# Kernel optimization log

Hardware: AMD Instinct MI355X
Metric: run time of the kernel (lower is better)

## Reference

```python
import jax, jax.numpy as jnp
import numpy as np

# Flattened-state gather indices. State is prev[9,3] flattened to 27 values,
# then concat with x -> flat[29], where flat[27]=a=x[0], flat[28]=b=x[1].
# Row t gives the (x0, x1, x2) inputs of triangle t, read from the source wiring.
IDX0 = np.array([3, 0, 6, 12, 9, 15, 18, 6, 15])   # x0 inputs
IDX1 = np.array([1, 7, 4, 19, 16, 13, 10, 22, 25])  # x1 inputs
IDX2 = np.array([17, 5, 11, 8, 28, 2, 27, 23, 26])  # x2 inputs (t=4 -> b, t=6 -> a)

NOISE_SCALE = 0.125  # LUT2 hard-codes noise = 0.125


def mux(s, a, b):
    return 0.5 * (s * b - s * a + a + b)


def setup_inputs() -> dict:
    key = jax.random.key(0)
    k1, k2, k3 = jax.random.split(key, 3)
    x = jax.random.normal(k1, (2,), dtype=jnp.float32)
    weights = jax.random.normal(k2, (9, 3, 4), dtype=jnp.float32)  # 9 triangles x 3 LUT2s x 4 weights
    noise = jax.random.normal(k3, (130, 9, 3, 4), dtype=jnp.float32)  # per-step np.random.normal draws
    return {"x": x, "weights": weights, "noise": noise, "dummy1": 0, "dummy2": 0}


def reference(x, weights, noise, dummy1, dummy2):
    del dummy1, dummy2  # unused in the original forward

    def step(prev, n):
        # prev: [9,3] current states; n: [9,3,4] noise for this step
        flat = jnp.concatenate([prev.reshape(-1), x])  # [29]
        x0, x1, x2 = flat[IDX0], flat[IDX1], flat[IDX2]  # each [9]
        # LUT j of each triangle: LUT0(x1,x2), LUT1(x0,x2), LUT2(x0,x1)
        A = jnp.stack([x1, x0, x0], axis=1)  # [9,3] first mux select
        B = jnp.stack([x2, x2, x1], axis=1)  # [9,3] second mux select
        w = weights + jnp.abs(1.0 - jnp.abs(weights)) * n * NOISE_SCALE  # [9,3,4]
        m0 = mux(A, w[..., 0], w[..., 1])
        m1 = mux(A, w[..., 2], w[..., 3])
        new = mux(B, m0, m1)  # [9,3] synchronous update (uupdate after all forwards)
        return new, None

    init = -jnp.ones((9, 3), dtype=x.dtype)  # all states start at -1
    final, _ = jax.lax.scan(step, init, noise)  # 130 steps
    return jnp.stack([final[0, 1], final[1, 2], final[7, 2]])
```

## Files before the change

kernel.cpp:

```cpp
#include <hip/hip_runtime.h>


#define STEPS 130
#define NLUT  27

__device__ __constant__ int c_idx0[9] = {3, 0, 6, 12, 9, 15, 18, 6, 15};
__device__ __constant__ int c_idx1[9] = {1, 7, 4, 19, 16, 13, 10, 22, 25};
__device__ __constant__ int c_idx2[9] = {17, 5, 11, 8, 28, 2, 27, 23, 26};

__global__ __launch_bounds__(1024)
void one_layer_net_kernel(const float* __restrict__ x,
                          const float* __restrict__ weights,
                          const float* __restrict__ noise,
                          float* __restrict__ out) {
    __shared__ float4 tbl[STEPS * NLUT];

    const int tid = threadIdx.x;

    const float4* __restrict__ w4 = (const float4*)weights;
    const float4* __restrict__ n4 = (const float4*)noise;
    for (int i = tid; i < STEPS * NLUT; i += 1024) {
        const int l = i % NLUT;
        float4 w = w4[l];
        float4 n = n4[i];
        float w0 = fmaf(fabsf(1.0f - fabsf(w.x)) * n.x, 0.125f, w.x);
        float w1 = fmaf(fabsf(1.0f - fabsf(w.y)) * n.y, 0.125f, w.y);
        float w2 = fmaf(fabsf(1.0f - fabsf(w.z)) * n.z, 0.125f, w.z);
        float w3 = fmaf(fabsf(1.0f - fabsf(w.w)) * n.w, 0.125f, w.w);
        tbl[i] = make_float4(0.5f * (w1 - w0), 0.5f * (w0 + w1),
                             0.5f * (w3 - w2), 0.5f * (w2 + w3));
    }
    __syncthreads();

    if (tid >= 64) return;

    const int l  = tid;
    const int lc = (l < NLUT) ? l : (NLUT - 1);
    const int t  = lc / 3;
    const int j  = lc % 3;
    const int srcA = (j == 0) ? c_idx1[t] : c_idx0[t];
    const int srcB = (j == 2) ? c_idx1[t] : c_idx2[t];

    float state = (l < NLUT) ? -1.0f
                : (l == 27)  ? x[0]
                : (l == 28)  ? x[1]
                : 0.0f;

    const float4* __restrict__ row = &tbl[lc];
    #pragma unroll 2
    for (int s = 0; s < STEPS; ++s) {
        float4 nf = row[s * NLUT];
        float gA = __shfl(state, srcA, 64);
        float gB = __shfl(state, srcB, 64);
        float m0 = fmaf(gA, nf.x, nf.y);
        float m1 = fmaf(gA, nf.z, nf.w);
        float nw = 0.5f * fmaf(gB, m1 - m0, m0 + m1);
        state = (l < NLUT) ? nw : state;
    }

    if (l == 1)  out[0] = state;
    if (l == 5)  out[1] = state;
    if (l == 23) out[2] = state;
}

extern "C" void kernel_launch(void* const* d_in, const int* in_sizes, int n_in,
                              void* d_out, int out_size, void* d_ws, size_t ws_size,
                              hipStream_t stream) {
    const float* x       = (const float*)d_in[0];
    const float* weights = (const float*)d_in[1];
    const float* noise   = (const float*)d_in[2];
    float* out = (float*)d_out;
    one_layer_net_kernel<<<1, 1024, 0, stream>>>(x, weights, noise, out);
}
```

Baseline: 67.33 us.

## Fold mux algebra into bilinear coefficients and fold constant inputs into the table

Rewrites each LUT update as a bilinear form K3*gA*gB + K2*gB + K1*gA + K0, precomputed per step in shared memory. This shortens the dependent chain per step from roughly four ops to two FMAs plus two permutes. LUTs that read the constant inputs a or b have those inputs folded into their coefficients, so the state lanes for x no longer need shuffling. The loop is also fully unrolled with the next step's coefficients prefetched, and it uses ds_bpermute directly. Full unrolling of 130 steps enlarges the code, and the reassociated arithmetic changes float rounding slightly.

```diff
diff --git a/kernel.cpp b/kernel.cpp
--- a/kernel.cpp
+++ b/kernel.cpp
@@ -16,6 +16,8 @@
     __shared__ float4 tbl[STEPS * NLUT];
 
     const int tid = threadIdx.x;
+    const float a = x[0];
+    const float b = x[1];
 
     const float4* __restrict__ w4 = (const float4*)weights;
     const float4* __restrict__ n4 = (const float4*)noise;
@@ -27,8 +29,19 @@
         float w1 = fmaf(fabsf(1.0f - fabsf(w.y)) * n.y, 0.125f, w.y);
         float w2 = fmaf(fabsf(1.0f - fabsf(w.z)) * n.z, 0.125f, w.z);
         float w3 = fmaf(fabsf(1.0f - fabsf(w.w)) * n.w, 0.125f, w.w);
-        tbl[i] = make_float4(0.5f * (w1 - w0), 0.5f * (w0 + w1),
-                             0.5f * (w3 - w2), 0.5f * (w2 + w3));
+        float d0 = w1 - w0, s0 = w0 + w1;
+        float d1 = w3 - w2, s1 = w2 + w3;
+        float K3 = 0.25f * (d1 - d0);
+        float K2 = 0.25f * (s1 - s0);
+        float K1 = 0.25f * (d0 + d1);
+        float K0 = 0.25f * (s0 + s1);
+        if (l == 12 || l == 13) {
+            K0 = fmaf(K2, b, K0); K1 = fmaf(K3, b, K1); K2 = 0.0f; K3 = 0.0f;
+        }
+        if (l == 18 || l == 19) {
+            K0 = fmaf(K2, a, K0); K1 = fmaf(K3, a, K1); K2 = 0.0f; K3 = 0.0f;
+        }
+        tbl[i] = make_float4(K3, K2, K1, K0);
     }
     __syncthreads();
 
@@ -38,24 +51,26 @@
     const int lc = (l < NLUT) ? l : (NLUT - 1);
     const int t  = lc / 3;
     const int j  = lc % 3;
-    const int srcA = (j == 0) ? c_idx1[t] : c_idx0[t];
-    const int srcB = (j == 2) ? c_idx1[t] : c_idx2[t];
+    int srcA = (j == 0) ? c_idx1[t] : c_idx0[t];
+    int srcB = (j == 2) ? c_idx1[t] : c_idx2[t];
+    if (srcB >= NLUT) srcB = 0;
+    const int bpA = srcA << 2;
+    const int bpB = srcB << 2;
 
-    float state = (l < NLUT) ? -1.0f
-                : (l == 27)  ? x[0]
-                : (l == 28)  ? x[1]
-                : 0.0f;
+    float state = -1.0f;
 
     const float4* __restrict__ row = &tbl[lc];
-    #pragma unroll 2
+    float4 k = row[0];
+    #pragma unroll
     for (int s = 0; s < STEPS; ++s) {
-        float4 nf = row[s * NLUT];
-        float gA = __shfl(state, srcA, 64);
-        float gB = __shfl(state, srcB, 64);
-        float m0 = fmaf(gA, nf.x, nf.y);
-        float m1 = fmaf(gA, nf.z, nf.w);
-        float nw = 0.5f * fmaf(gB, m1 - m0, m0 + m1);
-        state = (l < NLUT) ? nw : state;
+        const float4 kc = k;
+        if (s + 1 < STEPS) k = row[(s + 1) * NLUT];
+        const int si = __float_as_int(state);
+        const float gA = __int_as_float(__builtin_amdgcn_ds_bpermute(bpA, si));
+        const float gB = __int_as_float(__builtin_amdgcn_ds_bpermute(bpB, si));
+        const float t0 = fmaf(gA, kc.x, kc.y);
+        const float t1 = fmaf(gA, kc.z, kc.w);
+        state = fmaf(gB, t0, t1);
     }
 
     if (l == 1)  out[0] = state;
```

Result: faster. 65.37 us (-2.9%).
